# Performance work log

Measured on AMD Instinct MI355X. Metric: run time of the kernel, lower is better.

The kernel has to match this reference:

```python
import jax, jax.numpy as jnp
import numpy as np

HEADS = 4

def _proj(x, w, b):
    # 1x1 conv == per-pixel linear: x [B,C,H,W], w [O,C], b [O]
    return jnp.einsum('oc,bchw->bohw', w, x) + b[None, :, None, None]

def setup_inputs() -> dict:
    key = jax.random.key(0)
    ks = jax.random.split(key, 9)
    B, C, H, W = 16, 512, 32, 32
    emb = C // HEADS
    return {
        'x': jax.random.normal(ks[0], (B, C, H, W), jnp.float32),
        'wq_w': jax.random.normal(ks[1], (C, C), jnp.float32) * 0.02,
        'wq_b': jax.random.normal(ks[2], (C,), jnp.float32) * 0.02,
        'wk_w': jax.random.normal(ks[3], (C, C), jnp.float32) * 0.02,
        'wk_b': jax.random.normal(ks[4], (C,), jnp.float32) * 0.02,
        'wv_w': jax.random.normal(ks[5], (C, C), jnp.float32) * 0.02,
        'wv_b': jax.random.normal(ks[6], (C,), jnp.float32) * 0.02,
        'rh': jax.random.normal(ks[7], (1, HEADS, emb, 1, H), jnp.float32),
        'rw': jax.random.normal(ks[8], (1, HEADS, emb, W, 1), jnp.float32),
    }

def reference(x, wq_w, wq_b, wk_w, wk_b, wv_w, wv_b, rh, rw):
    B, C, H, W = x.shape
    heads = HEADS
    emb = C // heads
    scale = C ** (-0.5)
    N = H * W
    q = _proj(x, wq_w, wq_b).reshape(B, heads, emb, N).transpose(0, 1, 3, 2) * scale  # [B,h,N,d]
    kt = _proj(x, wk_w, wk_b).reshape(B, heads, emb, N)                               # [B,h,d,N]
    v = _proj(x, wv_w, wv_b).reshape(B, heads, emb, N).transpose(0, 1, 3, 2)          # [B,h,N,d]
    qkt = jnp.matmul(q, kt)                                                           # [B,h,N,N]
    # relative-position term: (rh + rw) broadcasts to [1,h,d,W,H], flattened as in source
    rt = (rh + rw).reshape(1, heads, emb, N)
    qrt = jnp.matmul(q, rt)                                                           # [B,h,N,N]
    attn = jax.nn.softmax(qkt + qrt, axis=-1)
    y = jnp.matmul(attn, v)                                                           # [B,h,N,d]
    return y.reshape(B, C, H, W)
```

## Files before the change

### kernel.cpp

```cpp
#include <hip/hip_runtime.h>
#include <hip/hip_bf16.h>
#include <cstdint>

#define NB 16
#define NC 512
#define NPIX 1024
#define NHEADS 4
#define NEMB 128

typedef short bf16x8 __attribute__((ext_vector_type(8)));
typedef float f32x4 __attribute__((ext_vector_type(4)));
typedef float f32x16 __attribute__((ext_vector_type(16)));
typedef unsigned short u16x4 __attribute__((ext_vector_type(4)));
typedef unsigned short u16x8 __attribute__((ext_vector_type(8)));

__device__ __forceinline__ unsigned short f2bf(float f) {
  union { float f; unsigned u; } c; c.f = f;
  return (unsigned short)((c.u + 0x7FFFu + ((c.u >> 16) & 1u)) >> 16);
}

__device__ __forceinline__ unsigned cvtpk_bf16(float lo, float hi) {
  unsigned r;
  asm("v_cvt_pk_bf16_f32 %0, %1, %2" : "=v"(r) : "v"(lo), "v"(hi));
  return r;
}

__device__ __forceinline__ void gload_lds16(const void* g, void* l) {
  __builtin_amdgcn_global_load_lds(
      (const __attribute__((address_space(1))) unsigned int*)g,
      (__attribute__((address_space(3))) unsigned int*)l, 16, 0, 0);
}

__global__ void k_prep(const float* __restrict__ x, unsigned short* __restrict__ xt,
                       const float* __restrict__ wq, const float* __restrict__ wk,
                       const float* __restrict__ wv, unsigned short* __restrict__ wb) {
  int bid = blockIdx.x;
  if (bid >= 2048) {
    int wbid = bid - 2048;
    for (int i = wbid * 256 + threadIdx.x; i < 3 * 65536; i += 256 * 256) {
      int p = i >> 16, idx = i & 65535;
      const float* src = p == 0 ? wq : (p == 1 ? wk : wv);
      float4 v = ((const float4*)src)[idx];
      u16x4 o = { f2bf(v.x), f2bf(v.y), f2bf(v.z), f2bf(v.w) };
      ((u16x4*)(wb + (size_t)p * NC * NC))[idx] = o;
    }
    return;
  }
  __shared__ float tile[4][32][33];
  int nt = bid & 31, ct4 = (bid >> 5) & 3, b = bid >> 7;
  int n0 = nt * 32, c0 = ct4 * 128;
  int t = threadIdx.x;
  int r = t >> 3, q = t & 7;
#pragma unroll
  for (int s = 0; s < 4; s++) {
    float4 v = *(const float4*)(x + ((size_t)(b * NC + c0 + s * 32 + r)) * NPIX + n0 + q * 4);
    tile[s][r][q * 4 + 0] = v.x; tile[s][r][q * 4 + 1] = v.y;
    tile[s][r][q * 4 + 2] = v.z; tile[s][r][q * 4 + 3] = v.w;
  }
  __syncthreads();
#pragma unroll
  for (int pass = 0; pass < 2; pass++) {
    int idx = pass * 256 + t;
    int n = idx >> 4;
    int c8 = (idx & 15) * 8;
    int s = c8 >> 5, cl = c8 & 31;
    u16x8 o;
#pragma unroll
    for (int j = 0; j < 8; j++) o[j] = f2bf(tile[s][cl + j][n]);
    *(u16x8*)(xt + ((size_t)(b * NPIX + n0 + n)) * NC + c0 + c8) = o;
  }
}

__global__ __launch_bounds__(256, 3) void k_qkv(
    const unsigned short* __restrict__ wb, const unsigned short* __restrict__ xt,
    const float* __restrict__ qb, const float* __restrict__ kb, const float* __restrict__ vb,
    const float* __restrict__ rh, const float* __restrict__ rw,
    unsigned short* __restrict__ Qs, unsigned short* __restrict__ Kn,
    unsigned short* __restrict__ Vm) {
  __shared__ __align__(16) char smem[32768];
  unsigned short* Alds = (unsigned short*)smem;
  unsigned short* Blds = (unsigned short*)(smem + 16384);
  int bid = blockIdx.x;
  int nt = bid & 7, mt = (bid >> 3) & 3;
  int rest = bid >> 5;
  int p = rest % 3, b = rest / 3;
  int m0 = mt * 128, n0 = nt * 128;
  const unsigned short* A = wb + (size_t)p * NC * NC + (size_t)m0 * NC;
  const unsigned short* Bx = xt + (size_t)b * NPIX * NC + (size_t)n0 * NC;
  int t = threadIdx.x;
  int lane = t & 63, wid = t >> 6;
  int wm = (wid >> 1) * 64, wn = (wid & 1) * 64;
  f32x4 acc[4][4] = {};
  for (int k0 = 0; k0 < NC; k0 += 64) {
#pragma unroll
    for (int i = 0; i < 4; i++) {
      int idx = i * 256 + t;
      int row = idx >> 3, col = (idx & 7) * 8;
      gload_lds16(A + (size_t)row * NC + k0 + col, &Alds[idx * 8]);
    }
#pragma unroll
    for (int i = 0; i < 4; i++) {
      int idx = i * 256 + t;
      int row = idx >> 3, col = (idx & 7) * 8;
      gload_lds16(Bx + (size_t)row * NC + k0 + col, &Blds[idx * 8]);
    }
    __syncthreads();
#pragma unroll
    for (int ks = 0; ks < 2; ks++) {
      int kk = ks * 32 + ((lane >> 4) << 3);
      bf16x8 af[4], bfr[4];
#pragma unroll
      for (int f = 0; f < 4; f++)
        af[f] = *(const bf16x8*)&Alds[(wm + f * 16 + (lane & 15)) * 64 + kk];
#pragma unroll
      for (int f = 0; f < 4; f++)
        bfr[f] = *(const bf16x8*)&Blds[(wn + f * 16 + (lane & 15)) * 64 + kk];
#pragma unroll
      for (int fm = 0; fm < 4; fm++)
#pragma unroll
        for (int fn = 0; fn < 4; fn++)
          acc[fm][fn] = __builtin_amdgcn_mfma_f32_16x16x32_bf16(af[fm], bfr[fn], acc[fm][fn], 0, 0, 0);
    }
    __syncthreads();
  }
  const float scale = 0.044194173824159216f * 1.4426950408889634f;
  if (p == 2) {
#pragma unroll
    for (int fm = 0; fm < 4; fm++) {
#pragma unroll
      for (int r = 0; r < 4; r++) {
        int d = wm + fm * 16 + ((lane >> 4) << 2) + r;
        float bv = vb[m0 + d];
#pragma unroll
        for (int fn = 0; fn < 4; fn++) {
          int jloc = wn + fn * 16 + (lane & 15);
          int sub = jloc >> 6, jl = jloc & 63;
          *(unsigned short*)(smem + sub * 16384 + d * 128 + ((2 * jl) ^ ((d & 7) << 4))) =
              f2bf(acc[fm][fn][r] + bv);
        }
      }
    }
  } else if (p == 1) {
#pragma unroll
    for (int fm = 0; fm < 4; fm++) {
      int e0 = wm + fm * 16 + ((lane >> 4) << 2);
#pragma unroll
      for (int fn = 0; fn < 4; fn++) {
        int jloc = wn + fn * 16 + (lane & 15);
        int jg = n0 + jloc;
        int sub = jloc >> 6, jl = jloc & 63;
        u16x4 o;
#pragma unroll
        for (int r = 0; r < 4; r++) {
          float v = acc[fm][fn][r] + kb[m0 + e0 + r];
          v += rh[(m0 + e0 + r) * 32 + (jg & 31)] + rw[(m0 + e0 + r) * 32 + (jg >> 5)];
          o[r] = f2bf(v);
        }
        *(u16x4*)(smem + sub * 16384 + jl * 256 + ((2 * e0) ^ ((jl & 7) << 4))) = o;
      }
    }
  } else {
#pragma unroll
    for (int fm = 0; fm < 4; fm++) {
      int e0 = wm + fm * 16 + ((lane >> 4) << 2);
#pragma unroll
      for (int fn = 0; fn < 4; fn++) {
        int ncol = wn + fn * 16 + (lane & 15);
        u16x4 o;
#pragma unroll
        for (int r = 0; r < 4; r++)
          o[r] = f2bf((acc[fm][fn][r] + qb[m0 + e0 + r]) * scale);
        *(u16x4*)(smem + ncol * 256 + 2 * e0) = o;
      }
    }
  }
  __syncthreads();
  char* gdst;
  if (p == 0)
    gdst = (char*)(Qs + ((size_t)((b * NHEADS + mt) * NPIX + n0)) * NEMB);
  else if (p == 1)
    gdst = (char*)(Kn + (size_t)(b * NHEADS + mt) * 131072 + (size_t)(n0 >> 6) * 8192);
  else
    gdst = (char*)(Vm + (size_t)(b * NHEADS + mt) * 131072 + (size_t)(n0 >> 6) * 8192);
#pragma unroll
  for (int i = 0; i < 8; i++)
    *(u16x8*)(gdst + i * 4096 + t * 16) = *(const u16x8*)(smem + i * 4096 + t * 16);
}

__global__ __launch_bounds__(256, 2) void k_attn(
    const unsigned short* __restrict__ Qs, const unsigned short* __restrict__ Kp,
    const unsigned short* __restrict__ Vp, float* __restrict__ out) {
  __shared__ __align__(16) char smem[65536];
  int bid = blockIdx.x;
  int pair = bid & 63;
  int b = pair >> 2, hd = pair & 3;
  int i0 = (bid >> 6) * 128;
  int t = threadIdx.x, w = t >> 6, lane = t & 63;
  int l31 = lane & 31, hi5 = lane >> 5;
  const unsigned short* Qb = Qs + (size_t)pair * NPIX * NEMB;
  const char* Kpb = (const char*)(Kp + (size_t)pair * 131072);
  const char* Vpb = (const char*)(Vp + (size_t)pair * 131072);

  bf16x8 qf[8];
  {
    const unsigned short* qr = Qb + (size_t)(i0 + w * 32 + l31) * NEMB + hi5 * 8;
#pragma unroll
    for (int d8 = 0; d8 < 8; d8++) qf[d8] = *(const bf16x8*)(qr + d8 * 16);
  }
  f32x16 yacc[4] = {};
  float l = 0.f;

#pragma unroll
  for (int r = 0; r < 4; r++) {
    gload_lds16(Kpb + r * 4096 + t * 16, smem + r * 4096 + t * 16);
    gload_lds16(Vpb + r * 4096 + t * 16, smem + 32768 + r * 4096 + t * 16);
  }
  __syncthreads();

  for (int tt = 0; tt < 16; tt++) {
    int cur = tt & 1;
    if (tt < 15) {
      const char* kn = Kpb + (tt + 1) * 16384;
      const char* vn = Vpb + (tt + 1) * 16384;
      char* kd = smem + (cur ^ 1) * 16384;
      char* vd = smem + 32768 + (cur ^ 1) * 16384;
#pragma unroll
      for (int r = 0; r < 4; r++) {
        gload_lds16(kn + r * 4096 + t * 16, kd + r * 4096 + t * 16);
        gload_lds16(vn + r * 4096 + t * 16, vd + r * 4096 + t * 16);
      }
    }
    const char* Kl = smem + cur * 16384;
    const char* Vl = smem + 32768 + cur * 16384;
    f32x16 sacc[2] = {};
    {
      int swz = (l31 & 7) << 4;
#pragma unroll
      for (int d8 = 0; d8 < 8; d8++) {
        int colb = (d8 * 32 + hi5 * 16) ^ swz;
        bf16x8 k0 = *(const bf16x8*)(Kl + l31 * 256 + colb);
        bf16x8 k1 = *(const bf16x8*)(Kl + (32 + l31) * 256 + colb);
        __builtin_amdgcn_s_setprio(1);
        sacc[0] = __builtin_amdgcn_mfma_f32_32x32x16_bf16(k0, qf[d8], sacc[0], 0, 0, 0);
        sacc[1] = __builtin_amdgcn_mfma_f32_32x32x16_bf16(k1, qf[d8], sacc[1], 0, 0, 0);
        __builtin_amdgcn_s_setprio(0);
      }
    }
    float rs0 = 0.f, rs1 = 0.f, rs2 = 0.f, rs3 = 0.f;
#pragma unroll
    for (int c = 0; c < 2; c++)
#pragma unroll
      for (int i = 0; i < 16; i += 4) {
        float p0 = exp2f(sacc[c][i + 0]);
        float p1 = exp2f(sacc[c][i + 1]);
        float p2 = exp2f(sacc[c][i + 2]);
        float p3 = exp2f(sacc[c][i + 3]);
        sacc[c][i + 0] = p0; sacc[c][i + 1] = p1;
        sacc[c][i + 2] = p2; sacc[c][i + 3] = p3;
        rs0 += p0; rs1 += p1; rs2 += p2; rs3 += p3;
      }
    l += (rs0 + rs1) + (rs2 + rs3);
    unsigned up[2][4][2];
#pragma unroll
    for (int c = 0; c < 2; c++)
#pragma unroll
      for (int g = 0; g < 4; g++) {
        up[c][g][0] = cvtpk_bf16(sacc[c][4 * g + 0], sacc[c][4 * g + 1]);
        up[c][g][1] = cvtpk_bf16(sacc[c][4 * g + 2], sacc[c][4 * g + 3]);
      }
    bf16x8 pf[4];
#pragma unroll
    for (int c2 = 0; c2 < 4; c2++) {
      int c = c2 >> 1, gA = (c2 & 1) * 2, gB = gA + 1;
      unsigned a0 = up[c][gA][0], b0 = up[c][gB][0];
      unsigned a1 = up[c][gA][1], b1 = up[c][gB][1];
      asm("v_permlane32_swap_b32 %0, %1" : "+v"(a0), "+v"(b0));
      asm("v_permlane32_swap_b32 %0, %1" : "+v"(a1), "+v"(b1));
      unsigned wd[4] = { a0, a1, b0, b1 };
      pf[c2] = *(bf16x8*)wd;
    }
    {
      int swz = (l31 & 7) << 4;
#pragma unroll
      for (int c2 = 0; c2 < 4; c2++) {
        int colb = (c2 * 32 + hi5 * 16) ^ swz;
        __builtin_amdgcn_s_setprio(1);
#pragma unroll
        for (int ds = 0; ds < 4; ds++) {
          bf16x8 vf = *(const bf16x8*)(Vl + (ds * 32 + l31) * 128 + colb);
          yacc[ds] = __builtin_amdgcn_mfma_f32_32x32x16_bf16(vf, pf[c2], yacc[ds], 0, 0, 0);
        }
        __builtin_amdgcn_s_setprio(0);
      }
    }
    __syncthreads();
  }
  float ltot = l + __shfl_xor(l, 32);
  float invl = 1.0f / ltot;
  int q = i0 + w * 32 + l31;
  float* orow = out + ((size_t)(b * NC + hd * NEMB + (q >> 3))) * NPIX + (q & 7) * NEMB;
#pragma unroll
  for (int ds = 0; ds < 4; ds++)
#pragma unroll
    for (int rg = 0; rg < 4; rg++) {
      f32x4 v;
#pragma unroll
      for (int i = 0; i < 4; i++) v[i] = yacc[ds][rg * 4 + i] * invl;
      *(f32x4*)(orow + ds * 32 + rg * 8 + hi5 * 4) = v;
    }
}

extern "C" void kernel_launch(void* const* d_in, const int* in_sizes, int n_in,
                              void* d_out, int out_size, void* d_ws, size_t ws_size,
                              hipStream_t stream) {
  const float* x  = (const float*)d_in[0];
  const float* wq = (const float*)d_in[1];
  const float* qb = (const float*)d_in[2];
  const float* wk = (const float*)d_in[3];
  const float* kb = (const float*)d_in[4];
  const float* wv = (const float*)d_in[5];
  const float* vb = (const float*)d_in[6];
  const float* rh = (const float*)d_in[7];
  const float* rw = (const float*)d_in[8];
  float* out = (float*)d_out;
  char* ws = (char*)d_ws;
  unsigned short* xt = (unsigned short*)(ws);
  unsigned short* wb = (unsigned short*)(ws + 16777216);
  unsigned short* Q  = (unsigned short*)(ws + 18350080);
  unsigned short* K  = (unsigned short*)(ws + 35127296);
  unsigned short* V  = (unsigned short*)(ws + 51904512);
  k_prep<<<2304, 256, 0, stream>>>(x, xt, wq, wk, wv, wb);
  k_qkv<<<1536, 256, 0, stream>>>(wb, xt, qb, kb, vb, rh, rw, Q, K, V);
  k_attn<<<512, 256, 0, stream>>>(Q, K, V, out);
}
```

Before: 101.9 us.

## Load V fragments directly from global into registers, halving attention LDS

The projection kernel now writes V in a fragment-ordered layout, so each lane's MFMA operand is one contiguous 16-byte global load. The attention kernel then reads V straight into registers each tile instead of staging it through double-buffered LDS, and the shared memory drops from 64KB to 32KB. This removes LDS traffic and bank pressure for V and may allow more resident blocks. The cost is 16 extra bf16x8 registers per tile and global-load latency that is only hidden if the loads are issued early enough, which the code tries by issuing them before the QK^T phase.

```diff
diff --git a/kernel.cpp b/kernel.cpp
--- a/kernel.cpp
+++ b/kernel.cpp
@@ -135,7 +135,9 @@
         for (int fn = 0; fn < 4; fn++) {
           int jloc = wn + fn * 16 + (lane & 15);
           int sub = jloc >> 6, jl = jloc & 63;
-          *(unsigned short*)(smem + sub * 16384 + d * 128 + ((2 * jl) ^ ((d & 7) << 4))) =
+          int c2 = jl >> 4, h5 = (jl >> 3) & 1, j8 = jl & 7;
+          *(unsigned short*)(smem + sub * 16384 +
+                             ((((c2 * 2 + h5) * 128 + d) * 8 + j8) * 2)) =
               f2bf(acc[fm][fn][r] + bv);
         }
       }
@@ -190,7 +192,7 @@
 __global__ __launch_bounds__(256, 2) void k_attn(
     const unsigned short* __restrict__ Qs, const unsigned short* __restrict__ Kp,
     const unsigned short* __restrict__ Vp, float* __restrict__ out) {
-  __shared__ __align__(16) char smem[65536];
+  __shared__ __align__(16) char smem[32768];
   int bid = blockIdx.x;
   int pair = bid & 63;
   int b = pair >> 2, hd = pair & 3;
@@ -199,7 +201,7 @@
   int l31 = lane & 31, hi5 = lane >> 5;
   const unsigned short* Qb = Qs + (size_t)pair * NPIX * NEMB;
   const char* Kpb = (const char*)(Kp + (size_t)pair * 131072);
-  const char* Vpb = (const char*)(Vp + (size_t)pair * 131072);
+  const unsigned short* Vg = Vp + (size_t)pair * 131072;
 
   bf16x8 qf[8];
   {
@@ -211,27 +213,27 @@
   float l = 0.f;
 
 #pragma unroll
-  for (int r = 0; r < 4; r++) {
+  for (int r = 0; r < 4; r++)
     gload_lds16(Kpb + r * 4096 + t * 16, smem + r * 4096 + t * 16);
-    gload_lds16(Vpb + r * 4096 + t * 16, smem + 32768 + r * 4096 + t * 16);
-  }
   __syncthreads();
 
   for (int tt = 0; tt < 16; tt++) {
     int cur = tt & 1;
+    bf16x8 vf[4][4];
+#pragma unroll
+    for (int c2 = 0; c2 < 4; c2++)
+#pragma unroll
+      for (int ds = 0; ds < 4; ds++)
+        vf[c2][ds] = *(const bf16x8*)(
+            Vg + ((((size_t)tt * 4 + c2) * 2 + hi5) * 128 + ds * 32 + l31) * 8);
     if (tt < 15) {
       const char* kn = Kpb + (tt + 1) * 16384;
-      const char* vn = Vpb + (tt + 1) * 16384;
       char* kd = smem + (cur ^ 1) * 16384;
-      char* vd = smem + 32768 + (cur ^ 1) * 16384;
-#pragma unroll
-      for (int r = 0; r < 4; r++) {
+#pragma unroll
+      for (int r = 0; r < 4; r++)
         gload_lds16(kn + r * 4096 + t * 16, kd + r * 4096 + t * 16);
-        gload_lds16(vn + r * 4096 + t * 16, vd + r * 4096 + t * 16);
-      }
     }
     const char* Kl = smem + cur * 16384;
-    const char* Vl = smem + 32768 + cur * 16384;
     f32x16 sacc[2] = {};
     {
       int swz = (l31 & 7) << 4;
@@ -279,20 +281,13 @@
       unsigned wd[4] = { a0, a1, b0, b1 };
       pf[c2] = *(bf16x8*)wd;
     }
-    {
-      int swz = (l31 & 7) << 4;
-#pragma unroll
-      for (int c2 = 0; c2 < 4; c2++) {
-        int colb = (c2 * 32 + hi5 * 16) ^ swz;
-        __builtin_amdgcn_s_setprio(1);
-#pragma unroll
-        for (int ds = 0; ds < 4; ds++) {
-          bf16x8 vf = *(const bf16x8*)(Vl + (ds * 32 + l31) * 128 + colb);
-          yacc[ds] = __builtin_amdgcn_mfma_f32_32x32x16_bf16(vf, pf[c2], yacc[ds], 0, 0, 0);
-        }
-        __builtin_amdgcn_s_setprio(0);
-      }
-    }
+    __builtin_amdgcn_s_setprio(1);
+#pragma unroll
+    for (int c2 = 0; c2 < 4; c2++)
+#pragma unroll
+      for (int ds = 0; ds < 4; ds++)
+        yacc[ds] = __builtin_amdgcn_mfma_f32_32x32x16_bf16(vf[c2][ds], pf[c2], yacc[ds], 0, 0, 0);
+    __builtin_amdgcn_s_setprio(0);
     __syncthreads();
   }
   float ltot = l + __shfl_xor(l, 32);
```

New measurement: 104.8 us. 1.03x slower.

## Software-pipeline attention loop so exp/PV of one half overlaps next QK chain

Applied to the files above, without the earlier changes.

Restructures the attention inner loop into a fully unrolled, two-stage software pipeline. The second 32-row half of each key tile is carried into the next iteration, so its exp/pack/PV work interleaves with the next tile's QK MFMA chain. V fragments are preloaded into registers. The aim is to hide the exp and permute latency behind matrix work instead of serialising QK, softmax and PV. In exchange it raises register pressure, since sA/sB and two V fragment sets stay live, which could spill or hurt occupancy at 2 blocks per CU. It also drops the setprio hints.

```diff
diff --git a/kernel.cpp b/kernel.cpp
--- a/kernel.cpp
+++ b/kernel.cpp
@@ -200,6 +200,7 @@
   const unsigned short* Qb = Qs + (size_t)pair * NPIX * NEMB;
   const char* Kpb = (const char*)(Kp + (size_t)pair * 131072);
   const char* Vpb = (const char*)(Vp + (size_t)pair * 131072);
+  const int swz = (l31 & 7) << 4;
 
   bf16x8 qf[8];
   {
@@ -217,84 +218,118 @@
   }
   __syncthreads();
 
-  for (int tt = 0; tt < 16; tt++) {
-    int cur = tt & 1;
-    if (tt < 15) {
-      const char* kn = Kpb + (tt + 1) * 16384;
-      const char* vn = Vpb + (tt + 1) * 16384;
-      char* kd = smem + (cur ^ 1) * 16384;
-      char* vd = smem + 32768 + (cur ^ 1) * 16384;
-#pragma unroll
-      for (int r = 0; r < 4; r++) {
-        gload_lds16(kn + r * 4096 + t * 16, kd + r * 4096 + t * 16);
-        gload_lds16(vn + r * 4096 + t * 16, vd + r * 4096 + t * 16);
-      }
-    }
-    const char* Kl = smem + cur * 16384;
-    const char* Vl = smem + 32768 + cur * 16384;
-    f32x16 sacc[2] = {};
-    {
-      int swz = (l31 & 7) << 4;
-#pragma unroll
-      for (int d8 = 0; d8 < 8; d8++) {
-        int colb = (d8 * 32 + hi5 * 16) ^ swz;
-        bf16x8 k0 = *(const bf16x8*)(Kl + l31 * 256 + colb);
-        bf16x8 k1 = *(const bf16x8*)(Kl + (32 + l31) * 256 + colb);
-        __builtin_amdgcn_s_setprio(1);
-        sacc[0] = __builtin_amdgcn_mfma_f32_32x32x16_bf16(k0, qf[d8], sacc[0], 0, 0, 0);
-        sacc[1] = __builtin_amdgcn_mfma_f32_32x32x16_bf16(k1, qf[d8], sacc[1], 0, 0, 0);
-        __builtin_amdgcn_s_setprio(0);
-      }
-    }
-    float rs0 = 0.f, rs1 = 0.f, rs2 = 0.f, rs3 = 0.f;
-#pragma unroll
-    for (int c = 0; c < 2; c++)
-#pragma unroll
-      for (int i = 0; i < 16; i += 4) {
-        float p0 = exp2f(sacc[c][i + 0]);
-        float p1 = exp2f(sacc[c][i + 1]);
-        float p2 = exp2f(sacc[c][i + 2]);
-        float p3 = exp2f(sacc[c][i + 3]);
-        sacc[c][i + 0] = p0; sacc[c][i + 1] = p1;
-        sacc[c][i + 2] = p2; sacc[c][i + 3] = p3;
-        rs0 += p0; rs1 += p1; rs2 += p2; rs3 += p3;
-      }
-    l += (rs0 + rs1) + (rs2 + rs3);
-    unsigned up[2][4][2];
-#pragma unroll
-    for (int c = 0; c < 2; c++)
-#pragma unroll
-      for (int g = 0; g < 4; g++) {
-        up[c][g][0] = cvtpk_bf16(sacc[c][4 * g + 0], sacc[c][4 * g + 1]);
-        up[c][g][1] = cvtpk_bf16(sacc[c][4 * g + 2], sacc[c][4 * g + 3]);
-      }
-    bf16x8 pf[4];
-#pragma unroll
-    for (int c2 = 0; c2 < 4; c2++) {
-      int c = c2 >> 1, gA = (c2 & 1) * 2, gB = gA + 1;
-      unsigned a0 = up[c][gA][0], b0 = up[c][gB][0];
-      unsigned a1 = up[c][gA][1], b1 = up[c][gB][1];
-      asm("v_permlane32_swap_b32 %0, %1" : "+v"(a0), "+v"(b0));
-      asm("v_permlane32_swap_b32 %0, %1" : "+v"(a1), "+v"(b1));
-      unsigned wd[4] = { a0, a1, b0, b1 };
-      pf[c2] = *(bf16x8*)wd;
-    }
-    {
-      int swz = (l31 & 7) << 4;
-#pragma unroll
-      for (int c2 = 0; c2 < 4; c2++) {
-        int colb = (c2 * 32 + hi5 * 16) ^ swz;
-        __builtin_amdgcn_s_setprio(1);
-#pragma unroll
-        for (int ds = 0; ds < 4; ds++) {
-          bf16x8 vf = *(const bf16x8*)(Vl + (ds * 32 + l31) * 128 + colb);
-          yacc[ds] = __builtin_amdgcn_mfma_f32_32x32x16_bf16(vf, pf[c2], yacc[ds], 0, 0, 0);
-        }
-        __builtin_amdgcn_s_setprio(0);
-      }
-    }
+#define PREFETCH(nt_, slot_)                                                    \
+  {                                                                             \
+    const char* kn = Kpb + (nt_) * 16384;                                       \
+    const char* vn = Vpb + (nt_) * 16384;                                       \
+    char* kd = smem + (slot_) * 16384;                                          \
+    char* vd = smem + 32768 + (slot_) * 16384;                                  \
+    _Pragma("unroll") for (int r = 0; r < 4; r++) {                             \
+      gload_lds16(kn + r * 4096 + t * 16, kd + r * 4096 + t * 16);              \
+      gload_lds16(vn + r * 4096 + t * 16, vd + r * 4096 + t * 16);              \
+    }                                                                           \
+  }
+
+#define CHAIN(S_, Kl_, roff_)                                                   \
+  _Pragma("unroll") for (int d8 = 0; d8 < 8; d8++) {                            \
+    int colb = (d8 * 32 + hi5 * 16) ^ swz;                                      \
+    bf16x8 kf = *(const bf16x8*)((Kl_) + (roff_ + l31) * 256 + colb);           \
+    S_ = __builtin_amdgcn_mfma_f32_32x32x16_bf16(kf, qf[d8], S_, 0, 0, 0);      \
+  }
+
+#define EXP_PACK_PV(S_, V_, rsum_)                                              \
+  {                                                                             \
+    _Pragma("unroll") for (int i = 0; i < 16; i += 4) {                         \
+      float p0 = exp2f(S_[i + 0]);                                              \
+      float p1 = exp2f(S_[i + 1]);                                              \
+      float p2 = exp2f(S_[i + 2]);                                              \
+      float p3 = exp2f(S_[i + 3]);                                              \
+      S_[i + 0] = p0; S_[i + 1] = p1; S_[i + 2] = p2; S_[i + 3] = p3;           \
+      rsum_ += (p0 + p1) + (p2 + p3);                                           \
+    }                                                                           \
+    unsigned uu[4][2];                                                          \
+    _Pragma("unroll") for (int g = 0; g < 4; g++) {                             \
+      uu[g][0] = cvtpk_bf16(S_[4 * g + 0], S_[4 * g + 1]);                      \
+      uu[g][1] = cvtpk_bf16(S_[4 * g + 2], S_[4 * g + 3]);                      \
+    }                                                                           \
+    _Pragma("unroll") for (int c2 = 0; c2 < 2; c2++) {                          \
+      int gA = c2 * 2, gB = gA + 1;                                             \
+      unsigned a0 = uu[gA][0], b0 = uu[gB][0];                                  \
+      unsigned a1 = uu[gA][1], b1 = uu[gB][1];                                  \
+      asm("v_permlane32_swap_b32 %0, %1" : "+v"(a0), "+v"(b0));                 \
+      asm("v_permlane32_swap_b32 %0, %1" : "+v"(a1), "+v"(b1));                 \
+      unsigned wd[4] = { a0, a1, b0, b1 };                                      \
+      bf16x8 pfx = *(bf16x8*)wd;                                                \
+      _Pragma("unroll") for (int ds = 0; ds < 4; ds++)                          \
+        yacc[ds] = __builtin_amdgcn_mfma_f32_32x32x16_bf16(V_[c2][ds], pfx,     \
+                                                           yacc[ds], 0, 0, 0); \
+    }                                                                           \
+  }
+
+#define VLOAD(V_, Vl_, cbase_)                                                  \
+  _Pragma("unroll") for (int c2 = 0; c2 < 2; c2++) {                            \
+    int colb = ((cbase_ + c2) * 32 + hi5 * 16) ^ swz;                           \
+    _Pragma("unroll") for (int ds = 0; ds < 4; ds++)                            \
+      V_[c2][ds] = *(const bf16x8*)((Vl_) + (ds * 32 + l31) * 128 + colb);      \
+  }
+
+  f32x16 sA, sB;
+  bf16x8 vAx[2][4], vBx[2][4];
+  float rsum = 0.f;
+
+  {
+    PREFETCH(1, 1);
+    const char* Kl = smem;
+    const char* Vl = smem + 32768;
+    f32x16 s0 = (f32x16)(0.0f);
+    CHAIN(s0, Kl, 0);
+    bf16x8 vloc[2][4];
+    VLOAD(vloc, Vl, 0);
+    VLOAD(vAx, Vl, 2);
+    sA = (f32x16)(0.0f);
+    CHAIN(sA, Kl, 32);
+    EXP_PACK_PV(s0, vloc, rsum);
     __syncthreads();
   }
+
+#define BODY(tt_, sin_, vin_, sout_, vout_, pre_)                               \
+  {                                                                             \
+    if (pre_) PREFETCH((tt_) + 1, ((tt_) & 1) ^ 1);                             \
+    const char* Kl = smem + ((tt_) & 1) * 16384;                                \
+    const char* Vl = smem + 32768 + ((tt_) & 1) * 16384;                        \
+    f32x16 s0 = (f32x16)(0.0f);                                                 \
+    CHAIN(s0, Kl, 0);                                                           \
+    EXP_PACK_PV(sin_, vin_, rsum);           \
+    bf16x8 vloc[2][4];                                                          \
+    VLOAD(vloc, Vl, 0);                                                         \
+    VLOAD(vout_, Vl, 2);                                                        \
+    sout_ = (f32x16)(0.0f);                                                     \
+    CHAIN(sout_, Kl, 32);                                                       \
+    EXP_PACK_PV(s0, vloc, rsum);                                                \
+    __syncthreads();                                                            \
+  }
+
+#pragma unroll
+  for (int i = 0; i < 7; i++) {
+    BODY(1 + 2 * i, sA, vAx, sB, vBx, true);
+    BODY(2 + 2 * i, sB, vBx, sA, vAx, true);
+  }
+  {
+    const char* Kl = smem + 16384;
+    const char* Vl = smem + 32768 + 16384;
+    f32x16 s0 = (f32x16)(0.0f);
+    CHAIN(s0, Kl, 0);
+    EXP_PACK_PV(sA, vAx, rsum);
+    bf16x8 vloc[2][4];
+    VLOAD(vloc, Vl, 0);
+    VLOAD(vBx, Vl, 2);
+    sB = (f32x16)(0.0f);
+    CHAIN(sB, Kl, 32);
+    EXP_PACK_PV(s0, vloc, rsum);
+    EXP_PACK_PV(sB, vBx, rsum);
+  }
+  l = rsum;
+
   float ltot = l + __shfl_xor(l, 32);
   float invl = 1.0f / ltot;
   int q = i0 + w * 32 + l31;
@@ -308,6 +343,11 @@
       for (int i = 0; i < 4; i++) v[i] = yacc[ds][rg * 4 + i] * invl;
       *(f32x4*)(orow + ds * 32 + rg * 8 + hi5 * 4) = v;
     }
+#undef PREFETCH
+#undef CHAIN
+#undef EXP_PACK_PV
+#undef VLOAD
+#undef BODY
 }
 
 extern "C" void kernel_launch(void* const* d_in, const int* in_sizes, int n_in,
```

After: 101.2 us. No clear change (-0.7%).
